# Kernel tuning notes

Measured on AMD Instinct MI355X. Metric: run time of the kernel, lower is better.

## Reference

```python
import jax, jax.numpy as jnp
import numpy as np

SIGMA = 1.0
S = 1.0 / (2.0 * SIGMA * SIGMA)  # 0.5


def setup_inputs() -> dict:
    key = jax.random.key(0)
    k1, k2 = jax.random.split(key)
    inputs = jax.random.normal(k1, (32, 4096, 3), dtype=jnp.float32)  # (B, N, D) point cloud
    # stars initialized RandomUniform(-1, 1) in the original build()
    stars = jax.random.uniform(k2, (1024, 3), minval=-1.0, maxval=1.0, dtype=jnp.float32)  # (M, D)
    return {"inputs": inputs, "stars": stars}


def reference(inputs, stars):
    # out[b, m] = sum_n exp(-S * ||inputs[b, n] - stars[m]||^2)
    # Use ||a-b||^2 = ||a||^2 - 2 a.b + ||b||^2 to avoid the (B, M, N, D) diff tensor.
    x2 = jnp.sum(inputs * inputs, axis=-1)          # (B, N)
    s2 = jnp.sum(stars * stars, axis=-1)            # (M,)
    cross = jnp.einsum('bnd,md->bmn', inputs, stars)  # (B, M, N)
    d2 = x2[:, None, :] - 2.0 * cross + s2[None, :, None]  # (B, M, N)
    return jnp.sum(jnp.exp(-S * d2), axis=2)        # (B, M)
```

## Files before the change

kernel.cpp:

```cpp
#include <hip/hip_runtime.h>


#define NB 32
#define NN 4096
#define NM 1024
#define NCHUNK 64
#define NPB (NN / NCHUNK)
#define TPB 256
#define MPT (NM / TPB)

__device__ __forceinline__ float exp2_hw(float x) {
    float r;
    asm("v_exp_f32 %0, %1" : "=v"(r) : "v"(x));
    return r;
}

__global__ __launch_bounds__(TPB, 8) void gau_part(const float* __restrict__ inputs,
                                                   const float* __restrict__ stars,
                                                   float* __restrict__ part) {
    constexpr float C2  = 0.72134752044448169f;
    constexpr float L2E = 1.44269504088896340f;

    const int b     = blockIdx.x / NCHUNK;
    const int chunk = blockIdx.x % NCHUNK;
    const int t     = threadIdx.x;

    __shared__ float4 pts[NPB];

    if (t < NPB) {
        const float* p = inputs + ((size_t)b * NN + (size_t)chunk * NPB + t) * 3;
        float x = p[0], y = p[1], z = p[2];
        float q = -C2 * x * x - C2 * y * y - C2 * z * z;
        pts[t] = make_float4(x, y, z, exp2_hw(q));
    }

    float Sx[MPT], Sy[MPT], Sz[MPT], K[MPT], acc[MPT];
#pragma unroll
    for (int k = 0; k < MPT; ++k) {
        int m = t + k * TPB;
        float sx = stars[3 * m + 0];
        float sy = stars[3 * m + 1];
        float sz = stars[3 * m + 2];
        Sx[k] = L2E * sx;
        Sy[k] = L2E * sy;
        Sz[k] = L2E * sz;
        K[k]  = -C2 * (sx * sx + sy * sy + sz * sz);
        acc[k] = 0.0f;
    }

    __syncthreads();

#pragma unroll 8
    for (int i = 0; i < NPB; ++i) {
        float4 p = pts[i];
#pragma unroll
        for (int k = 0; k < MPT; ++k) {
            float u = fmaf(p.z, Sz[k], K[k]);
            u = fmaf(p.y, Sy[k], u);
            u = fmaf(p.x, Sx[k], u);
            acc[k] = fmaf(p.w, exp2_hw(u), acc[k]);
        }
    }

    float* pb = part + ((size_t)b * NCHUNK + chunk) * NM;
#pragma unroll
    for (int k = 0; k < MPT; ++k) {
        pb[t + k * TPB] = acc[k];
    }
}

__global__ __launch_bounds__(256) void gau_reduce(const float* __restrict__ part,
                                                  float* __restrict__ out) {
    const int o = blockIdx.x * 256 + threadIdx.x;
    const int b = o >> 10;
    const int m = o & (NM - 1);
    const float* pb = part + (size_t)b * NCHUNK * NM + m;
    float s = 0.0f;
#pragma unroll
    for (int c = 0; c < NCHUNK; ++c) {
        s += pb[(size_t)c * NM];
    }
    out[o] = s;
}

extern "C" void kernel_launch(void* const* d_in, const int* in_sizes, int n_in,
                              void* d_out, int out_size, void* d_ws, size_t ws_size,
                              hipStream_t stream) {
    const float* inputs = (const float*)d_in[0];
    const float* stars  = (const float*)d_in[1];
    float* out  = (float*)d_out;
    float* part = (float*)d_ws;

    gau_part<<<NB * NCHUNK, TPB, 0, stream>>>(inputs, stars, part);
    gau_reduce<<<(NB * NM) / 256, 256, 0, stream>>>(part, out);
}
```

Before: 32.75 us.

## Increase stars per thread and split points across waves with LDS combine

```diff
diff --git a/kernel.cpp b/kernel.cpp
--- a/kernel.cpp
+++ b/kernel.cpp
@@ -2,12 +2,11 @@
 
 
 #define NB 32
-#define NN 4096
-#define NM 1024
-#define NCHUNK 64
-#define NPB (NN / NCHUNK)
-#define TPB 256
-#define MPT (NM / TPB)
+#define NBLK 32
+#define NPB 128
+#define NPW 64
+#define TPB 128
+#define MPT 16
 
 __device__ __forceinline__ float exp2_hw(float x) {
     float r;
@@ -15,20 +14,23 @@
     return r;
 }
 
-__global__ __launch_bounds__(TPB, 8) void gau_part(const float* __restrict__ inputs,
+__global__ __launch_bounds__(TPB, 2) void gau_part(const float* __restrict__ inputs,
                                                    const float* __restrict__ stars,
                                                    float* __restrict__ part) {
     constexpr float C2  = 0.72134752044448169f;
     constexpr float L2E = 1.44269504088896340f;
 
-    const int b     = blockIdx.x / NCHUNK;
-    const int chunk = blockIdx.x % NCHUNK;
-    const int t     = threadIdx.x;
+    const int b    = blockIdx.x / NBLK;
+    const int blk  = blockIdx.x % NBLK;
+    const int t    = threadIdx.x;
+    const int wave = t >> 6;
+    const int lane = t & 63;
 
     __shared__ float4 pts[NPB];
+    __shared__ float  part_lds[1024];
 
-    if (t < NPB) {
-        const float* p = inputs + ((size_t)b * NN + (size_t)chunk * NPB + t) * 3;
+    {
+        const float* p = inputs + ((size_t)b * 4096 + (size_t)blk * NPB + t) * 3;
         float x = p[0], y = p[1], z = p[2];
         float q = -C2 * x * x - C2 * y * y - C2 * z * z;
         pts[t] = make_float4(x, y, z, exp2_hw(q));
@@ -37,7 +39,7 @@
     float Sx[MPT], Sy[MPT], Sz[MPT], K[MPT], acc[MPT];
 #pragma unroll
     for (int k = 0; k < MPT; ++k) {
-        int m = t + k * TPB;
+        int m = lane * MPT + k;
         float sx = stars[3 * m + 0];
         float sy = stars[3 * m + 1];
         float sz = stars[3 * m + 2];
@@ -50,9 +52,10 @@
 
     __syncthreads();
 
-#pragma unroll 8
-    for (int i = 0; i < NPB; ++i) {
-        float4 p = pts[i];
+    const int pbase = wave * NPW;
+#pragma unroll 4
+    for (int i = 0; i < NPW; ++i) {
+        float4 p = pts[pbase + i];
 #pragma unroll
         for (int k = 0; k < MPT; ++k) {
             float u = fmaf(p.z, Sz[k], K[k]);
@@ -62,10 +65,25 @@
         }
     }
 
-    float* pb = part + ((size_t)b * NCHUNK + chunk) * NM;
+    if (wave == 1) {
 #pragma unroll
-    for (int k = 0; k < MPT; ++k) {
-        pb[t + k * TPB] = acc[k];
+        for (int c = 0; c < MPT / 4; ++c) {
+            *(float4*)&part_lds[lane * MPT + 4 * c] =
+                make_float4(acc[4 * c], acc[4 * c + 1], acc[4 * c + 2], acc[4 * c + 3]);
+        }
+    }
+    __syncthreads();
+    if (wave == 0) {
+        float* prow = part + (size_t)blockIdx.x * 1024;
+#pragma unroll
+        for (int c = 0; c < MPT / 4; ++c) {
+            float4 o = *(float4*)&part_lds[lane * MPT + 4 * c];
+            o.x += acc[4 * c];
+            o.y += acc[4 * c + 1];
+            o.z += acc[4 * c + 2];
+            o.w += acc[4 * c + 3];
+            *(float4*)&prow[lane * MPT + 4 * c] = o;
+        }
     }
 }
 
@@ -73,12 +91,12 @@
                                                   float* __restrict__ out) {
     const int o = blockIdx.x * 256 + threadIdx.x;
     const int b = o >> 10;
-    const int m = o & (NM - 1);
-    const float* pb = part + (size_t)b * NCHUNK * NM + m;
+    const int m = o & 1023;
+    const float* pb = part + (size_t)b * NBLK * 1024 + m;
     float s = 0.0f;
 #pragma unroll
-    for (int c = 0; c < NCHUNK; ++c) {
-        s += pb[(size_t)c * NM];
+    for (int c = 0; c < NBLK; ++c) {
+        s += pb[(size_t)c * 1024];
     }
     out[o] = s;
 }
@@ -91,6 +109,6 @@
     float* out  = (float*)d_out;
     float* part = (float*)d_ws;
 
-    gau_part<<<NB * NCHUNK, TPB, 0, stream>>>(inputs, stars, part);
-    gau_reduce<<<(NB * NM) / 256, 256, 0, stream>>>(part, out);
+    gau_part<<<NB * NBLK, TPB, 0, stream>>>(inputs, stars, part);
+    gau_reduce<<<(NB * 1024) / 256, 256, 0, stream>>>(part, out);
 }
```

New measurement: 32.35 us. Within noise of the previous version (-1.2%).
